# Performance work log

Hardware: AMD Instinct MI355X
Metric: run time of the kernel (lower is better)

Reference implementation:

```python
import jax, jax.numpy as jnp
import numpy as np

B, N, C, D = 16, 1024, 768, 384

def setup_inputs() -> dict:
    key = jax.random.key(0)
    ks = jax.random.split(key, 12)
    s_in = 1.0 / np.sqrt(C)
    s_d = 1.0 / np.sqrt(D)
    return {
        "x": jax.random.normal(ks[0], (B, N, C), dtype=jnp.float32),
        "adj": jax.random.uniform(ks[1], (B, N, N), dtype=jnp.float32),
        "W_theta": jax.random.uniform(ks[2], (C, D), minval=-s_in, maxval=s_in),
        "b_theta": jax.random.uniform(ks[3], (D,), minval=-s_in, maxval=s_in),
        "W_phi": jax.random.uniform(ks[4], (C, D), minval=-s_in, maxval=s_in),
        "b_phi": jax.random.uniform(ks[5], (D,), minval=-s_in, maxval=s_in),
        "W_g": jax.random.uniform(ks[6], (C, D), minval=-s_in, maxval=s_in),
        "b_g": jax.random.uniform(ks[7], (D,), minval=-s_in, maxval=s_in),
        "W_out": jax.random.uniform(ks[8], (D, C), minval=-s_d, maxval=s_d),
        "b_out": jax.random.uniform(ks[9], (C,), minval=-s_d, maxval=s_d),
    }

def reference(x, adj, W_theta, b_theta, W_phi, b_phi, W_g, b_g, W_out, b_out):
    # projections: [B,N,C] @ [C,D] -> [B,N,D]
    theta = x @ W_theta + b_theta
    phi = x @ W_phi + b_phi
    g = x @ W_g + b_g
    # unscaled attention scores with multiplicative adjacency mask
    attn = jnp.einsum('bnd,bmd->bnm', theta, phi) * adj  # [B,N,N]
    attn = jax.nn.softmax(attn, axis=-1)  # dropout is identity in eval mode
    out = jnp.einsum('bnm,bmd->bnd', attn, g)  # [B,N,D]
    out = out @ W_out + b_out  # [B,N,C]
    return out + x
```

## Files before the change

### kernel.cpp

```cpp
#include <hip/hip_runtime.h>
#include <hip/hip_bf16.h>

typedef __hip_bfloat16 bf16;
typedef short bf16x8 __attribute__((ext_vector_type(8)));
typedef float f32x4 __attribute__((ext_vector_type(4)));

constexpr int Bb = 16, Nn = 1024, Cc = 768, Dd = 384;

static __device__ __forceinline__ f32x4 mfma16(bf16x8 a, bf16x8 b, f32x4 c) {
    return __builtin_amdgcn_mfma_f32_16x16x32_bf16(a, b, c, 0, 0, 0);
}
static __device__ __forceinline__ short f2b(float v) {
    __hip_bfloat16 h = __float2bfloat16(v);
    return *reinterpret_cast<short*>(&h);
}
static __device__ __forceinline__ float b2f(bf16 x) { return __bfloat162float(x); }
static __device__ __forceinline__ float ldf(const float* p) { return *p; }
static __device__ __forceinline__ float ldf(const bf16* p) { return __bfloat162float(*p); }

__global__ __launch_bounds__(256) void transpose_cast(
    const float* __restrict__ in, bf16* __restrict__ out, int K, int N)
{
    __shared__ float t[32][33];
    const int n0 = blockIdx.x * 32, k0 = blockIdx.y * 32;
    const int tx = threadIdx.x & 31, ty = threadIdx.x >> 5;
#pragma unroll
    for (int i = 0; i < 4; i++)
        t[ty + i * 8][tx] = in[(size_t)(k0 + ty + i * 8) * N + n0 + tx];
    __syncthreads();
#pragma unroll
    for (int i = 0; i < 4; i++)
        out[(size_t)(n0 + ty + i * 8) * K + k0 + tx] = __float2bfloat16(t[tx][ty + i * 8]);
}

template <typename TA, int EPI>
__global__ __launch_bounds__(256) void gemm_mfma(
    const TA* __restrict__ A, const bf16* __restrict__ BT,
    const float* __restrict__ bias, const float* __restrict__ resid,
    void* __restrict__ outp, int K, int Nout)
{
    __shared__ short As[128 * 40];
    __shared__ short Bs[128 * 40];
    const int tid = threadIdx.x;
    const int lane = tid & 63, w = tid >> 6;
    const int quad = lane >> 4, c = lane & 15;
    const int row0 = blockIdx.x * 128, col0 = blockIdx.y * 128;
    const int wm = (w & 1) * 64, wn = (w >> 1) * 64;

    const f32x4 fz = {0.f, 0.f, 0.f, 0.f};
    f32x4 acc[4][4];
#pragma unroll
    for (int i = 0; i < 4; i++)
#pragma unroll
        for (int j = 0; j < 4; j++) acc[i][j] = fz;

    for (int k0 = 0; k0 < K; k0 += 32) {
        __syncthreads();
        if (sizeof(TA) == 4) {
            const float* Af = (const float*)A;
#pragma unroll
            for (int u = 0; u < 4; u++) {
                const int id = u * 256 + tid;
                const int r = id >> 3, c4 = (id & 7) * 4;
                const float4 v = *reinterpret_cast<const float4*>(Af + (size_t)(row0 + r) * K + k0 + c4);
                uint2 p;
                p.x = ((unsigned)(unsigned short)f2b(v.y) << 16) | (unsigned short)(unsigned)f2b(v.x);
                p.y = ((unsigned)(unsigned short)f2b(v.w) << 16) | (unsigned short)(unsigned)f2b(v.z);
                *reinterpret_cast<uint2*>(&As[r * 40 + c4]) = p;
            }
        } else {
            const bf16* Ab = (const bf16*)A;
#pragma unroll
            for (int u = 0; u < 2; u++) {
                const int id = u * 256 + tid;
                const int r = id >> 2, c8 = (id & 3) * 8;
                const uint4 v = *reinterpret_cast<const uint4*>(Ab + (size_t)(row0 + r) * K + k0 + c8);
                *reinterpret_cast<uint4*>(&As[r * 40 + c8]) = v;
            }
        }
#pragma unroll
        for (int u = 0; u < 2; u++) {
            const int id = u * 256 + tid;
            const int r = id >> 2, c8 = (id & 3) * 8;
            const uint4 v = *reinterpret_cast<const uint4*>(BT + (size_t)(col0 + r) * K + k0 + c8);
            *reinterpret_cast<uint4*>(&Bs[r * 40 + c8]) = v;
        }
        __syncthreads();

        bf16x8 af[4], bfr[4];
#pragma unroll
        for (int i = 0; i < 4; i++)
            af[i] = *reinterpret_cast<const bf16x8*>(&As[(wm + i * 16 + c) * 40 + quad * 8]);
#pragma unroll
        for (int j = 0; j < 4; j++)
            bfr[j] = *reinterpret_cast<const bf16x8*>(&Bs[(wn + j * 16 + c) * 40 + quad * 8]);
#pragma unroll
        for (int i = 0; i < 4; i++)
#pragma unroll
            for (int j = 0; j < 4; j++)
                acc[i][j] = mfma16(af[i], bfr[j], acc[i][j]);
    }

#pragma unroll
    for (int i = 0; i < 4; i++) {
        const int rowb = row0 + wm + i * 16 + quad * 4;
#pragma unroll
        for (int j = 0; j < 4; j++) {
            const int col = col0 + wn + j * 16 + c;
            const float bcol = bias[col];
#pragma unroll
            for (int r = 0; r < 4; r++) {
                float v = acc[i][j][r] + bcol;
                const int rr = rowb + r;
                if (EPI == 0) {
                    ((bf16*)outp)[(size_t)rr * Nout + col] = __float2bfloat16(v);
                } else if (EPI == 1) {
                    const int bb = rr >> 10, m = rr & 1023;
                    ((bf16*)outp)[((size_t)(bb * Nout + col)) * 1024 + m] = __float2bfloat16(v);
                } else {
                    v += resid[(size_t)rr * Nout + col];
                    ((float*)outp)[(size_t)rr * Nout + col] = v;
                }
            }
        }
    }
}

__global__ __launch_bounds__(256) void flash_attn(
    const bf16* __restrict__ theta, const bf16* __restrict__ phi,
    const bf16* __restrict__ gT, const float* __restrict__ adj,
    bf16* __restrict__ O)
{
    __shared__ short phs[32 * 392];
    __shared__ short gts[384 * 40];
    __shared__ short pls[4][16 * 40];

    const int tid = threadIdx.x;
    const int lane = tid & 63, w = tid >> 6;
    const int quad = lane >> 4, c = lane & 15;
    const int qb = blockIdx.x, b = blockIdx.y;

    const size_t thbase = ((size_t)b * Nn + qb * 64 + w * 16 + c) * Dd;
    bf16x8 ath[12];
#pragma unroll
    for (int dq = 0; dq < 12; dq++)
        ath[dq] = *reinterpret_cast<const bf16x8*>(theta + thbase + dq * 32 + quad * 8);

    const f32x4 fz = {0.f, 0.f, 0.f, 0.f};
    f32x4 o[24];
#pragma unroll
    for (int t = 0; t < 24; t++) o[t] = fz;
    float mrow[4], lrow[4];
#pragma unroll
    for (int r = 0; r < 4; r++) { mrow[r] = -INFINITY; lrow[r] = 0.f; }

    for (int n0 = 0; n0 < Nn; n0 += 32) {
        __syncthreads();
        {
            const bf16* src = phi + ((size_t)b * Nn + n0) * Dd;
#pragma unroll
            for (int u = 0; u < 6; u++) {
                const int id = u * 256 + tid;
                const int r = id / 48, cc = (id % 48) * 8;
                const uint4 v = *reinterpret_cast<const uint4*>(src + (size_t)r * Dd + cc);
                *reinterpret_cast<uint4*>(&phs[r * 392 + cc]) = v;
            }
        }
        {
            const bf16* src = gT + ((size_t)b * Dd) * Nn + n0;
#pragma unroll
            for (int u = 0; u < 6; u++) {
                const int id = u * 256 + tid;
                const int r = id >> 2, cc = (id & 3) * 8;
                const uint4 v = *reinterpret_cast<const uint4*>(src + (size_t)r * Nn + cc);
                *reinterpret_cast<uint4*>(&gts[r * 40 + cc]) = v;
            }
        }
        __syncthreads();

        f32x4 s0 = fz, s1 = fz;
#pragma unroll
        for (int dq = 0; dq < 12; dq++) {
            const bf16x8 b0 = *reinterpret_cast<const bf16x8*>(&phs[c * 392 + dq * 32 + quad * 8]);
            const bf16x8 b1 = *reinterpret_cast<const bf16x8*>(&phs[(16 + c) * 392 + dq * 32 + quad * 8]);
            s0 = mfma16(ath[dq], b0, s0);
            s1 = mfma16(ath[dq], b1, s1);
        }

        const float* arow = adj + ((size_t)b * Nn + qb * 64 + w * 16 + quad * 4) * Nn + n0;
        float p0[4], p1[4], alpha[4];
#pragma unroll
        for (int r = 0; r < 4; r++) {
            const float v0 = s0[r] * arow[(size_t)r * Nn + c];
            const float v1 = s1[r] * arow[(size_t)r * Nn + 16 + c];
            float t = fmaxf(v0, v1);
#pragma unroll
            for (int msk = 1; msk < 16; msk <<= 1) t = fmaxf(t, __shfl_xor(t, msk));
            const float mn = fmaxf(mrow[r], t);
            alpha[r] = __expf(mrow[r] - mn);
            mrow[r] = mn;
            p0[r] = __expf(v0 - mn);
            p1[r] = __expf(v1 - mn);
            float u = p0[r] + p1[r];
#pragma unroll
            for (int msk = 1; msk < 16; msk <<= 1) u += __shfl_xor(u, msk);
            lrow[r] = lrow[r] * alpha[r] + u;
        }
#pragma unroll
        for (int t = 0; t < 24; t++)
#pragma unroll
            for (int r = 0; r < 4; r++) o[t][r] *= alpha[r];

        short* pl = (short*)pls[w];
#pragma unroll
        for (int r = 0; r < 4; r++) {
            pl[(quad * 4 + r) * 40 + c] = f2b(p0[r]);
            pl[(quad * 4 + r) * 40 + 16 + c] = f2b(p1[r]);
        }
        __syncthreads();
        const bf16x8 ap = *reinterpret_cast<const bf16x8*>(&pl[c * 40 + quad * 8]);
#pragma unroll
        for (int dn = 0; dn < 24; dn++) {
            const bf16x8 bg = *reinterpret_cast<const bf16x8*>(&gts[(dn * 16 + c) * 40 + quad * 8]);
            o[dn] = mfma16(ap, bg, o[dn]);
        }
    }

    float inv[4];
#pragma unroll
    for (int r = 0; r < 4; r++) inv[r] = 1.0f / lrow[r];
    bf16* orow = O + ((size_t)b * Nn + qb * 64 + w * 16 + quad * 4) * Dd;
#pragma unroll
    for (int dn = 0; dn < 24; dn++)
#pragma unroll
        for (int r = 0; r < 4; r++)
            orow[(size_t)r * Dd + dn * 16 + c] = __float2bfloat16(o[dn][r] * inv[r]);
}

__global__ __launch_bounds__(256) void proj_gemm(
    const float* __restrict__ A, const float* __restrict__ W,
    const float* __restrict__ bias, bf16* __restrict__ out,
    int M, int K, int Nd)
{
    __shared__ float Asm[16][65];
    __shared__ float Bsm[16][65];
    const int tid = threadIdx.x;
    const int tx = tid & 15, ty = tid >> 4;
    const int row0 = blockIdx.x * 64, col0 = blockIdx.y * 64;
    float acc[4][4] = {};
    for (int k0 = 0; k0 < K; k0 += 16) {
        {
            const int m = tid >> 2, kq = (tid & 3) * 4;
            const float* p = A + (size_t)(row0 + m) * K + k0 + kq;
#pragma unroll
            for (int j = 0; j < 4; j++) Asm[kq + j][m] = p[j];
        }
        {
            const int k = tid >> 4, n4 = (tid & 15) * 4;
            const float* p = W + (size_t)(k0 + k) * Nd + col0 + n4;
#pragma unroll
            for (int j = 0; j < 4; j++) Bsm[k][n4 + j] = p[j];
        }
        __syncthreads();
#pragma unroll
        for (int k = 0; k < 16; k++) {
            float a[4], bv[4];
#pragma unroll
            for (int j = 0; j < 4; j++) a[j] = Asm[k][ty * 4 + j];
#pragma unroll
            for (int j = 0; j < 4; j++) bv[j] = Bsm[k][tx * 4 + j];
#pragma unroll
            for (int i = 0; i < 4; i++)
#pragma unroll
                for (int j = 0; j < 4; j++) acc[i][j] += a[i] * bv[j];
        }
        __syncthreads();
    }
#pragma unroll
    for (int i = 0; i < 4; i++) {
        const int row = row0 + ty * 4 + i;
#pragma unroll
        for (int j = 0; j < 4; j++) {
            const int col = col0 + tx * 4 + j;
            out[(size_t)row * Nd + col] = __float2bfloat16(acc[i][j] + bias[col]);
        }
    }
}

__global__ __launch_bounds__(256) void fused_attn(
    const float* __restrict__ x, const float* __restrict__ adj,
    const float* __restrict__ W_theta, const float* __restrict__ b_theta,
    const bf16* __restrict__ phi, const bf16* __restrict__ g,
    const float* __restrict__ W_out, const float* __restrict__ b_out,
    float* __restrict__ out)
{
    __shared__ float xs[Cc];
    __shared__ float th[Dd];
    __shared__ float s[Nn];
    __shared__ float Os[Dd];
    __shared__ float red[256];
    const int tid = threadIdx.x;
    const int n = blockIdx.x, b = blockIdx.y;
    const int lane = tid & 63, wave = tid >> 6;
    const size_t row = (size_t)b * Nn + n;
    const size_t baseD = (size_t)b * Nn * Dd;
    for (int c = tid; c < Cc; c += 256) xs[c] = x[row * Cc + c];
    __syncthreads();
    for (int d = tid; d < Dd; d += 256) {
        float acc = b_theta[d];
#pragma unroll 8
        for (int c = 0; c < Cc; c++) acc += xs[c] * W_theta[(size_t)c * Dd + d];
        th[d] = acc;
    }
    __syncthreads();
    for (int m = wave; m < Nn; m += 4) {
        const bf16* prow = phi + baseD + (size_t)m * Dd;
        float partial = 0.f;
#pragma unroll
        for (int j = 0; j < 6; j++) {
            const int d = lane + 64 * j;
            partial += th[d] * b2f(prow[d]);
        }
#pragma unroll
        for (int off = 32; off > 0; off >>= 1) partial += __shfl_down(partial, off);
        if (lane == 0)
            s[m] = partial * adj[(size_t)b * Nn * Nn + (size_t)n * Nn + m];
    }
    __syncthreads();
    float mx = -1e30f;
    for (int i = tid; i < Nn; i += 256) mx = fmaxf(mx, s[i]);
    red[tid] = mx; __syncthreads();
    for (int st = 128; st > 0; st >>= 1) {
        if (tid < st) red[tid] = fmaxf(red[tid], red[tid + st]);
        __syncthreads();
    }
    mx = red[0]; __syncthreads();
    float lsum = 0.f;
    for (int i = tid; i < Nn; i += 256) {
        const float e = __expf(s[i] - mx);
        s[i] = e;
        lsum += e;
    }
    red[tid] = lsum; __syncthreads();
    for (int st = 128; st > 0; st >>= 1) {
        if (tid < st) red[tid] += red[tid + st];
        __syncthreads();
    }
    const float inv = 1.0f / red[0];
    __syncthreads();
    for (int d = tid; d < Dd; d += 256) {
        float acc = 0.f;
#pragma unroll 8
        for (int m = 0; m < Nn; m++) acc += s[m] * b2f(g[baseD + (size_t)m * Dd + d]);
        Os[d] = acc * inv;
    }
    __syncthreads();
    for (int c = tid; c < Cc; c += 256) {
        float acc = b_out[c] + xs[c];
#pragma unroll 8
        for (int d = 0; d < Dd; d++) acc += Os[d] * W_out[(size_t)d * Cc + c];
        out[row * Cc + c] = acc;
    }
}

extern "C" void kernel_launch(void* const* d_in, const int* in_sizes, int n_in,
                              void* d_out, int out_size, void* d_ws, size_t ws_size,
                              hipStream_t stream)
{
    const float* x       = (const float*)d_in[0];
    const float* adj     = (const float*)d_in[1];
    const float* W_theta = (const float*)d_in[2];
    const float* b_theta = (const float*)d_in[3];
    const float* W_phi   = (const float*)d_in[4];
    const float* b_phi   = (const float*)d_in[5];
    const float* W_g     = (const float*)d_in[6];
    const float* b_g     = (const float*)d_in[7];
    const float* W_out   = (const float*)d_in[8];
    const float* b_out   = (const float*)d_in[9];
    float* out = (float*)d_out;

    const int M = Bb * Nn;
    const size_t SZ = (size_t)Bb * Nn * Dd;
    const size_t WSZ = (size_t)Cc * Dd;
    const size_t NEED = (4 * WSZ + 4 * SZ) * sizeof(bf16);

    dim3 blk(256);

    if (ws_size >= NEED) {
        bf16* WtT   = (bf16*)d_ws;
        bf16* WpT   = WtT + WSZ;
        bf16* WgT   = WpT + WSZ;
        bf16* WoT   = WgT + WSZ;
        bf16* theta = WoT + WSZ;
        bf16* phi   = theta + SZ;
        bf16* gT    = phi + SZ;
        bf16* O     = gT + SZ;

        transpose_cast<<<dim3(Dd / 32, Cc / 32), blk, 0, stream>>>(W_theta, WtT, Cc, Dd);
        transpose_cast<<<dim3(Dd / 32, Cc / 32), blk, 0, stream>>>(W_phi,   WpT, Cc, Dd);
        transpose_cast<<<dim3(Dd / 32, Cc / 32), blk, 0, stream>>>(W_g,     WgT, Cc, Dd);
        transpose_cast<<<dim3(Cc / 32, Dd / 32), blk, 0, stream>>>(W_out,   WoT, Dd, Cc);

        dim3 gp(M / 128, Dd / 128);
        gemm_mfma<float, 0><<<gp, blk, 0, stream>>>(x, WtT, b_theta, nullptr, theta, Cc, Dd);
        gemm_mfma<float, 0><<<gp, blk, 0, stream>>>(x, WpT, b_phi,   nullptr, phi,   Cc, Dd);
        gemm_mfma<float, 1><<<gp, blk, 0, stream>>>(x, WgT, b_g,     nullptr, gT,    Cc, Dd);

        flash_attn<<<dim3(Nn / 64, Bb), blk, 0, stream>>>(theta, phi, gT, adj, O);

        dim3 go(M / 128, Cc / 128);
        gemm_mfma<bf16, 2><<<go, blk, 0, stream>>>(O, WoT, b_out, x, out, Dd, Cc);
    } else {
        bf16* phi = (bf16*)d_ws;
        bf16* g   = phi + SZ;
        dim3 gproj(M / 64, Dd / 64);
        proj_gemm<<<gproj, blk, 0, stream>>>(x, W_phi, b_phi, phi, M, Cc, Dd);
        proj_gemm<<<gproj, blk, 0, stream>>>(x, W_g, b_g, g, M, Cc, Dd);
        fused_attn<<<dim3(Nn, Bb), blk, 0, stream>>>(
            x, adj, W_theta, b_theta, phi, g, W_out, b_out, out);
    }
}
```

Baseline: 377.2 us.

## Fuse projections, double-buffer phi via async LDS loads, read gT from global

The three projection GEMMs become one launch over a concatenated 1152-wide weight, so x is read and converted once, and the three weight transposes become one launch. In attention, phi tiles are double-buffered in LDS with swizzled direct global-to-LDS loads, and adj is loaded before the score MFMAs. The gT tile staging and one barrier per iteration are dropped, so gT is read straight from global memory. The O output overwrites theta in place and the fallback path is removed, which assumes the workspace is always large enough.

```diff
diff --git a/kernel.cpp b/kernel.cpp
--- a/kernel.cpp
+++ b/kernel.cpp
@@ -14,37 +14,57 @@
     __hip_bfloat16 h = __float2bfloat16(v);
     return *reinterpret_cast<short*>(&h);
 }
-static __device__ __forceinline__ float b2f(bf16 x) { return __bfloat162float(x); }
-static __device__ __forceinline__ float ldf(const float* p) { return *p; }
-static __device__ __forceinline__ float ldf(const bf16* p) { return __bfloat162float(*p); }
-
-__global__ __launch_bounds__(256) void transpose_cast(
-    const float* __restrict__ in, bf16* __restrict__ out, int K, int N)
+static __device__ __forceinline__ void ld16(void* lds, const void* g) {
+    __builtin_amdgcn_global_load_lds(
+        (const __attribute__((address_space(1))) unsigned int*)g,
+        (__attribute__((address_space(3))) unsigned int*)lds, 16, 0, 0);
+}
+
+__global__ __launch_bounds__(256) void transpose_proj(
+    const float* __restrict__ W0, const float* __restrict__ W1,
+    const float* __restrict__ W2, bf16* __restrict__ out)
+{
+    __shared__ float t[32][33];
+    const float* in = blockIdx.z == 0 ? W0 : blockIdx.z == 1 ? W1 : W2;
+    bf16* o = out + (size_t)blockIdx.z * Dd * Cc;
+    const int n0 = blockIdx.x * 32, k0 = blockIdx.y * 32;
+    const int tx = threadIdx.x & 31, ty = threadIdx.x >> 5;
+#pragma unroll
+    for (int i = 0; i < 4; i++)
+        t[ty + i * 8][tx] = in[(size_t)(k0 + ty + i * 8) * Dd + n0 + tx];
+    __syncthreads();
+#pragma unroll
+    for (int i = 0; i < 4; i++)
+        o[(size_t)(n0 + ty + i * 8) * Cc + k0 + tx] = __float2bfloat16(t[tx][ty + i * 8]);
+}
+
+__global__ __launch_bounds__(256) void transpose_wout(
+    const float* __restrict__ in, bf16* __restrict__ out)
 {
     __shared__ float t[32][33];
     const int n0 = blockIdx.x * 32, k0 = blockIdx.y * 32;
     const int tx = threadIdx.x & 31, ty = threadIdx.x >> 5;
 #pragma unroll
     for (int i = 0; i < 4; i++)
-        t[ty + i * 8][tx] = in[(size_t)(k0 + ty + i * 8) * N + n0 + tx];
+        t[ty + i * 8][tx] = in[(size_t)(k0 + ty + i * 8) * Cc + n0 + tx];
     __syncthreads();
 #pragma unroll
     for (int i = 0; i < 4; i++)
-        out[(size_t)(n0 + ty + i * 8) * K + k0 + tx] = __float2bfloat16(t[tx][ty + i * 8]);
-}
-
-template <typename TA, int EPI>
-__global__ __launch_bounds__(256) void gemm_mfma(
-    const TA* __restrict__ A, const bf16* __restrict__ BT,
-    const float* __restrict__ bias, const float* __restrict__ resid,
-    void* __restrict__ outp, int K, int Nout)
+        out[(size_t)(n0 + ty + i * 8) * Dd + k0 + tx] = __float2bfloat16(t[tx][ty + i * 8]);
+}
+
+__global__ __launch_bounds__(256) void gemm_proj(
+    const float* __restrict__ A, const bf16* __restrict__ BT,
+    const float* __restrict__ b_t, const float* __restrict__ b_p,
+    const float* __restrict__ b_gv,
+    bf16* __restrict__ th, bf16* __restrict__ ph, bf16* __restrict__ gt)
 {
     __shared__ short As[128 * 40];
     __shared__ short Bs[128 * 40];
     const int tid = threadIdx.x;
     const int lane = tid & 63, w = tid >> 6;
     const int quad = lane >> 4, c = lane & 15;
-    const int row0 = blockIdx.x * 128, col0 = blockIdx.y * 128;
+    const int col0 = blockIdx.x * 128, row0 = blockIdx.y * 128;
     const int wm = (w & 1) * 64, wn = (w >> 1) * 64;
 
     const f32x4 fz = {0.f, 0.f, 0.f, 0.f};
@@ -54,35 +74,100 @@
 #pragma unroll
         for (int j = 0; j < 4; j++) acc[i][j] = fz;
 
-    for (int k0 = 0; k0 < K; k0 += 32) {
-        __syncthreads();
-        if (sizeof(TA) == 4) {
-            const float* Af = (const float*)A;
-#pragma unroll
-            for (int u = 0; u < 4; u++) {
-                const int id = u * 256 + tid;
-                const int r = id >> 3, c4 = (id & 7) * 4;
-                const float4 v = *reinterpret_cast<const float4*>(Af + (size_t)(row0 + r) * K + k0 + c4);
-                uint2 p;
-                p.x = ((unsigned)(unsigned short)f2b(v.y) << 16) | (unsigned short)(unsigned)f2b(v.x);
-                p.y = ((unsigned)(unsigned short)f2b(v.w) << 16) | (unsigned short)(unsigned)f2b(v.z);
-                *reinterpret_cast<uint2*>(&As[r * 40 + c4]) = p;
-            }
-        } else {
-            const bf16* Ab = (const bf16*)A;
-#pragma unroll
-            for (int u = 0; u < 2; u++) {
-                const int id = u * 256 + tid;
-                const int r = id >> 2, c8 = (id & 3) * 8;
-                const uint4 v = *reinterpret_cast<const uint4*>(Ab + (size_t)(row0 + r) * K + k0 + c8);
-                *reinterpret_cast<uint4*>(&As[r * 40 + c8]) = v;
-            }
+    for (int k0 = 0; k0 < Cc; k0 += 32) {
+        __syncthreads();
+#pragma unroll
+        for (int u = 0; u < 4; u++) {
+            const int id = u * 256 + tid;
+            const int r = id >> 3, c4 = (id & 7) * 4;
+            const float4 v = *reinterpret_cast<const float4*>(A + (size_t)(row0 + r) * Cc + k0 + c4);
+            uint2 p;
+            p.x = ((unsigned)(unsigned short)f2b(v.y) << 16) | (unsigned short)(unsigned)f2b(v.x);
+            p.y = ((unsigned)(unsigned short)f2b(v.w) << 16) | (unsigned short)(unsigned)f2b(v.z);
+            *reinterpret_cast<uint2*>(&As[r * 40 + c4]) = p;
         }
 #pragma unroll
         for (int u = 0; u < 2; u++) {
             const int id = u * 256 + tid;
             const int r = id >> 2, c8 = (id & 3) * 8;
-            const uint4 v = *reinterpret_cast<const uint4*>(BT + (size_t)(col0 + r) * K + k0 + c8);
+            const uint4 v = *reinterpret_cast<const uint4*>(BT + (size_t)(col0 + r) * Cc + k0 + c8);
+            *reinterpret_cast<uint4*>(&Bs[r * 40 + c8]) = v;
+        }
+        __syncthreads();
+
+        bf16x8 af[4], bfr[4];
+#pragma unroll
+        for (int i = 0; i < 4; i++)
+            af[i] = *reinterpret_cast<const bf16x8*>(&As[(wm + i * 16 + c) * 40 + quad * 8]);
+#pragma unroll
+        for (int j = 0; j < 4; j++)
+            bfr[j] = *reinterpret_cast<const bf16x8*>(&Bs[(wn + j * 16 + c) * 40 + quad * 8]);
+#pragma unroll
+        for (int i = 0; i < 4; i++)
+#pragma unroll
+            for (int j = 0; j < 4; j++)
+                acc[i][j] = mfma16(af[i], bfr[j], acc[i][j]);
+    }
+
+    const int sel = col0 >= 768 ? 2 : (col0 >= 384 ? 1 : 0);
+    const float* bp = sel == 0 ? b_t : sel == 1 ? b_p : b_gv;
+    bf16* dst = sel == 0 ? th : sel == 1 ? ph : gt;
+    const int cbase = sel * 384;
+#pragma unroll
+    for (int i = 0; i < 4; i++) {
+        const int rowb = row0 + wm + i * 16 + quad * 4;
+#pragma unroll
+        for (int j = 0; j < 4; j++) {
+            const int col = col0 + wn + j * 16 + c;
+            const int cl = col - cbase;
+            const float bcol = bp[cl];
+#pragma unroll
+            for (int r = 0; r < 4; r++) {
+                const float v = acc[i][j][r] + bcol;
+                const int rr = rowb + r;
+                if (sel < 2)
+                    dst[(size_t)rr * 384 + cl] = __float2bfloat16(v);
+                else
+                    dst[((size_t)((rr >> 10) * 384 + cl) << 10) + (rr & 1023)] = __float2bfloat16(v);
+            }
+        }
+    }
+}
+
+__global__ __launch_bounds__(256) void gemm_out(
+    const bf16* __restrict__ A, const bf16* __restrict__ BT,
+    const float* __restrict__ bias, const float* __restrict__ resid,
+    float* __restrict__ out)
+{
+    __shared__ short As[128 * 40];
+    __shared__ short Bs[128 * 40];
+    const int tid = threadIdx.x;
+    const int lane = tid & 63, w = tid >> 6;
+    const int quad = lane >> 4, c = lane & 15;
+    const int col0 = blockIdx.x * 128, row0 = blockIdx.y * 128;
+    const int wm = (w & 1) * 64, wn = (w >> 1) * 64;
+
+    const f32x4 fz = {0.f, 0.f, 0.f, 0.f};
+    f32x4 acc[4][4];
+#pragma unroll
+    for (int i = 0; i < 4; i++)
+#pragma unroll
+        for (int j = 0; j < 4; j++) acc[i][j] = fz;
+
+    for (int k0 = 0; k0 < Dd; k0 += 32) {
+        __syncthreads();
+#pragma unroll
+        for (int u = 0; u < 2; u++) {
+            const int id = u * 256 + tid;
+            const int r = id >> 2, c8 = (id & 3) * 8;
+            const uint4 v = *reinterpret_cast<const uint4*>(A + (size_t)(row0 + r) * Dd + k0 + c8);
+            *reinterpret_cast<uint4*>(&As[r * 40 + c8]) = v;
+        }
+#pragma unroll
+        for (int u = 0; u < 2; u++) {
+            const int id = u * 256 + tid;
+            const int r = id >> 2, c8 = (id & 3) * 8;
+            const uint4 v = *reinterpret_cast<const uint4*>(BT + (size_t)(col0 + r) * Dd + k0 + c8);
             *reinterpret_cast<uint4*>(&Bs[r * 40 + c8]) = v;
         }
         __syncthreads();
@@ -110,29 +195,18 @@
             const float bcol = bias[col];
 #pragma unroll
             for (int r = 0; r < 4; r++) {
-                float v = acc[i][j][r] + bcol;
                 const int rr = rowb + r;
-                if (EPI == 0) {
-                    ((bf16*)outp)[(size_t)rr * Nout + col] = __float2bfloat16(v);
-                } else if (EPI == 1) {
-                    const int bb = rr >> 10, m = rr & 1023;
-                    ((bf16*)outp)[((size_t)(bb * Nout + col)) * 1024 + m] = __float2bfloat16(v);
-                } else {
-                    v += resid[(size_t)rr * Nout + col];
-                    ((float*)outp)[(size_t)rr * Nout + col] = v;
-                }
+                out[(size_t)rr * Cc + col] = acc[i][j][r] + bcol + resid[(size_t)rr * Cc + col];
             }
         }
     }
 }
 
-__global__ __launch_bounds__(256) void flash_attn(
-    const bf16* __restrict__ theta, const bf16* __restrict__ phi,
-    const bf16* __restrict__ gT, const float* __restrict__ adj,
-    bf16* __restrict__ O)
-{
-    __shared__ short phs[32 * 392];
-    __shared__ short gts[384 * 40];
+__global__ __launch_bounds__(256) void flash_attn2(
+    bf16* __restrict__ thetaO, const bf16* __restrict__ phi,
+    const bf16* __restrict__ gT, const float* __restrict__ adj)
+{
+    __shared__ char phs[2][24576];
     __shared__ short pls[4][16 * 40];
 
     const int tid = threadIdx.x;
@@ -140,11 +214,14 @@
     const int quad = lane >> 4, c = lane & 15;
     const int qb = blockIdx.x, b = blockIdx.y;
 
+    const bf16* phi_b = phi + (size_t)b * Nn * Dd;
+    const bf16* gT_b  = gT + (size_t)b * Dd * Nn;
+
     const size_t thbase = ((size_t)b * Nn + qb * 64 + w * 16 + c) * Dd;
     bf16x8 ath[12];
 #pragma unroll
     for (int dq = 0; dq < 12; dq++)
-        ath[dq] = *reinterpret_cast<const bf16x8*>(theta + thbase + dq * 32 + quad * 8);
+        ath[dq] = *reinterpret_cast<const bf16x8*>(thetaO + thbase + dq * 32 + quad * 8);
 
     const f32x4 fz = {0.f, 0.f, 0.f, 0.f};
     f32x4 o[24];
@@ -154,45 +231,56 @@
 #pragma unroll
     for (int r = 0; r < 4; r++) { mrow[r] = -INFINITY; lrow[r] = 0.f; }
 
-    for (int n0 = 0; n0 < Nn; n0 += 32) {
-        __syncthreads();
-        {
-            const bf16* src = phi + ((size_t)b * Nn + n0) * Dd;
-#pragma unroll
-            for (int u = 0; u < 6; u++) {
-                const int id = u * 256 + tid;
-                const int r = id / 48, cc = (id % 48) * 8;
-                const uint4 v = *reinterpret_cast<const uint4*>(src + (size_t)r * Dd + cc);
-                *reinterpret_cast<uint4*>(&phs[r * 392 + cc]) = v;
-            }
-        }
-        {
-            const bf16* src = gT + ((size_t)b * Dd) * Nn + n0;
-#pragma unroll
-            for (int u = 0; u < 6; u++) {
-                const int id = u * 256 + tid;
-                const int r = id >> 2, cc = (id & 3) * 8;
-                const uint4 v = *reinterpret_cast<const uint4*>(src + (size_t)r * Nn + cc);
-                *reinterpret_cast<uint4*>(&gts[r * 40 + cc]) = v;
-            }
-        }
-        __syncthreads();
+    {
+        char* dst = phs[0];
+#pragma unroll
+        for (int t = 0; t < 6; t++) {
+            const int op = w * 6 + t;
+            const int gc = op * 64 + lane;
+            const int r = gc / 48, j = gc - r * 48;
+            ld16(dst + op * 1024, phi_b + (size_t)r * Dd + ((j ^ (r & 7)) << 3));
+        }
+    }
+
+    for (int ci = 0; ci < 32; ci++) {
+        const int n0 = ci * 32;
+        __syncthreads();
+        const char* buf = phs[ci & 1];
+
+        const float* arow = adj + ((size_t)b * Nn + qb * 64 + w * 16 + quad * 4) * Nn + n0;
+        float a0[4], a1[4];
+#pragma unroll
+        for (int r = 0; r < 4; r++) {
+            a0[r] = arow[(size_t)r * Nn + c];
+            a1[r] = arow[(size_t)r * Nn + 16 + c];
+        }
 
         f32x4 s0 = fz, s1 = fz;
 #pragma unroll
         for (int dq = 0; dq < 12; dq++) {
-            const bf16x8 b0 = *reinterpret_cast<const bf16x8*>(&phs[c * 392 + dq * 32 + quad * 8]);
-            const bf16x8 b1 = *reinterpret_cast<const bf16x8*>(&phs[(16 + c) * 392 + dq * 32 + quad * 8]);
+            const int sw = ((dq * 4 + quad) ^ (c & 7)) << 4;
+            const bf16x8 b0 = *reinterpret_cast<const bf16x8*>(buf + c * 768 + sw);
+            const bf16x8 b1 = *reinterpret_cast<const bf16x8*>(buf + (16 + c) * 768 + sw);
             s0 = mfma16(ath[dq], b0, s0);
             s1 = mfma16(ath[dq], b1, s1);
         }
 
-        const float* arow = adj + ((size_t)b * Nn + qb * 64 + w * 16 + quad * 4) * Nn + n0;
+        if (ci < 31) {
+            char* dst = phs[(ci + 1) & 1];
+#pragma unroll
+            for (int t = 0; t < 6; t++) {
+                const int op = w * 6 + t;
+                const int gc = op * 64 + lane;
+                const int r = gc / 48, j = gc - r * 48;
+                ld16(dst + op * 1024, phi_b + (size_t)(n0 + 32 + r) * Dd + ((j ^ (r & 7)) << 3));
+            }
+        }
+
         float p0[4], p1[4], alpha[4];
 #pragma unroll
         for (int r = 0; r < 4; r++) {
-            const float v0 = s0[r] * arow[(size_t)r * Nn + c];
-            const float v1 = s1[r] * arow[(size_t)r * Nn + 16 + c];
+            const float v0 = s0[r] * a0[r];
+            const float v1 = s1[r] * a1[r];
             float t = fmaxf(v0, v1);
 #pragma unroll
             for (int msk = 1; msk < 16; msk <<= 1) t = fmaxf(t, __shfl_xor(t, msk));
@@ -217,11 +305,12 @@
             pl[(quad * 4 + r) * 40 + c] = f2b(p0[r]);
             pl[(quad * 4 + r) * 40 + 16 + c] = f2b(p1[r]);
         }
-        __syncthreads();
         const bf16x8 ap = *reinterpret_cast<const bf16x8*>(&pl[c * 40 + quad * 8]);
+
 #pragma unroll
         for (int dn = 0; dn < 24; dn++) {
-            const bf16x8 bg = *reinterpret_cast<const bf16x8*>(&gts[(dn * 16 + c) * 40 + quad * 8]);
+            const bf16x8 bg = *reinterpret_cast<const bf16x8*>(
+                gT_b + (size_t)(dn * 16 + c) * Nn + n0 + quad * 8);
             o[dn] = mfma16(ap, bg, o[dn]);
         }
     }
@@ -229,138 +318,12 @@
     float inv[4];
 #pragma unroll
     for (int r = 0; r < 4; r++) inv[r] = 1.0f / lrow[r];
-    bf16* orow = O + ((size_t)b * Nn + qb * 64 + w * 16 + quad * 4) * Dd;
+    bf16* orow = thetaO + ((size_t)b * Nn + qb * 64 + w * 16 + quad * 4) * Dd;
 #pragma unroll
     for (int dn = 0; dn < 24; dn++)
 #pragma unroll
         for (int r = 0; r < 4; r++)
             orow[(size_t)r * Dd + dn * 16 + c] = __float2bfloat16(o[dn][r] * inv[r]);
-}
-
-__global__ __launch_bounds__(256) void proj_gemm(
-    const float* __restrict__ A, const float* __restrict__ W,
-    const float* __restrict__ bias, bf16* __restrict__ out,
-    int M, int K, int Nd)
-{
-    __shared__ float Asm[16][65];
-    __shared__ float Bsm[16][65];
-    const int tid = threadIdx.x;
-    const int tx = tid & 15, ty = tid >> 4;
-    const int row0 = blockIdx.x * 64, col0 = blockIdx.y * 64;
-    float acc[4][4] = {};
-    for (int k0 = 0; k0 < K; k0 += 16) {
-        {
-            const int m = tid >> 2, kq = (tid & 3) * 4;
-            const float* p = A + (size_t)(row0 + m) * K + k0 + kq;
-#pragma unroll
-            for (int j = 0; j < 4; j++) Asm[kq + j][m] = p[j];
-        }
-        {
-            const int k = tid >> 4, n4 = (tid & 15) * 4;
-            const float* p = W + (size_t)(k0 + k) * Nd + col0 + n4;
-#pragma unroll
-            for (int j = 0; j < 4; j++) Bsm[k][n4 + j] = p[j];
-        }
-        __syncthreads();
-#pragma unroll
-        for (int k = 0; k < 16; k++) {
-            float a[4], bv[4];
-#pragma unroll
-            for (int j = 0; j < 4; j++) a[j] = Asm[k][ty * 4 + j];
-#pragma unroll
-            for (int j = 0; j < 4; j++) bv[j] = Bsm[k][tx * 4 + j];
-#pragma unroll
-            for (int i = 0; i < 4; i++)
-#pragma unroll
-                for (int j = 0; j < 4; j++) acc[i][j] += a[i] * bv[j];
-        }
-        __syncthreads();
-    }
-#pragma unroll
-    for (int i = 0; i < 4; i++) {
-        const int row = row0 + ty * 4 + i;
-#pragma unroll
-        for (int j = 0; j < 4; j++) {
-            const int col = col0 + tx * 4 + j;
-            out[(size_t)row * Nd + col] = __float2bfloat16(acc[i][j] + bias[col]);
-        }
-    }
-}
-
-__global__ __launch_bounds__(256) void fused_attn(
-    const float* __restrict__ x, const float* __restrict__ adj,
-    const float* __restrict__ W_theta, const float* __restrict__ b_theta,
-    const bf16* __restrict__ phi, const bf16* __restrict__ g,
-    const float* __restrict__ W_out, const float* __restrict__ b_out,
-    float* __restrict__ out)
-{
-    __shared__ float xs[Cc];
-    __shared__ float th[Dd];
-    __shared__ float s[Nn];
-    __shared__ float Os[Dd];
-    __shared__ float red[256];
-    const int tid = threadIdx.x;
-    const int n = blockIdx.x, b = blockIdx.y;
-    const int lane = tid & 63, wave = tid >> 6;
-    const size_t row = (size_t)b * Nn + n;
-    const size_t baseD = (size_t)b * Nn * Dd;
-    for (int c = tid; c < Cc; c += 256) xs[c] = x[row * Cc + c];
-    __syncthreads();
-    for (int d = tid; d < Dd; d += 256) {
-        float acc = b_theta[d];
-#pragma unroll 8
-        for (int c = 0; c < Cc; c++) acc += xs[c] * W_theta[(size_t)c * Dd + d];
-        th[d] = acc;
-    }
-    __syncthreads();
-    for (int m = wave; m < Nn; m += 4) {
-        const bf16* prow = phi + baseD + (size_t)m * Dd;
-        float partial = 0.f;
-#pragma unroll
-        for (int j = 0; j < 6; j++) {
-            const int d = lane + 64 * j;
-            partial += th[d] * b2f(prow[d]);
-        }
-#pragma unroll
-        for (int off = 32; off > 0; off >>= 1) partial += __shfl_down(partial, off);
-        if (lane == 0)
-            s[m] = partial * adj[(size_t)b * Nn * Nn + (size_t)n * Nn + m];
-    }
-    __syncthreads();
-    float mx = -1e30f;
-    for (int i = tid; i < Nn; i += 256) mx = fmaxf(mx, s[i]);
-    red[tid] = mx; __syncthreads();
-    for (int st = 128; st > 0; st >>= 1) {
-        if (tid < st) red[tid] = fmaxf(red[tid], red[tid + st]);
-        __syncthreads();
-    }
-    mx = red[0]; __syncthreads();
-    float lsum = 0.f;
-    for (int i = tid; i < Nn; i += 256) {
-        const float e = __expf(s[i] - mx);
-        s[i] = e;
-        lsum += e;
-    }
-    red[tid] = lsum; __syncthreads();
-    for (int st = 128; st > 0; st >>= 1) {
-        if (tid < st) red[tid] += red[tid + st];
-        __syncthreads();
-    }
-    const float inv = 1.0f / red[0];
-    __syncthreads();
-    for (int d = tid; d < Dd; d += 256) {
-        float acc = 0.f;
-#pragma unroll 8
-        for (int m = 0; m < Nn; m++) acc += s[m] * b2f(g[baseD + (size_t)m * Dd + d]);
-        Os[d] = acc * inv;
-    }
-    __syncthreads();
-    for (int c = tid; c < Cc; c += 256) {
-        float acc = b_out[c] + xs[c];
-#pragma unroll 8
-        for (int d = 0; d < Dd; d++) acc += Os[d] * W_out[(size_t)d * Cc + c];
-        out[row * Cc + c] = acc;
-    }
 }
 
 extern "C" void kernel_launch(void* const* d_in, const int* in_sizes, int n_in,
@@ -379,44 +342,24 @@
     const float* b_out   = (const float*)d_in[9];
     float* out = (float*)d_out;
 
-    const int M = Bb * Nn;
-    const size_t SZ = (size_t)Bb * Nn * Dd;
+    const size_t SZ  = (size_t)Bb * Nn * Dd;
     const size_t WSZ = (size_t)Cc * Dd;
-    const size_t NEED = (4 * WSZ + 4 * SZ) * sizeof(bf16);
+
+    bf16* WT_all = (bf16*)d_ws;
+    bf16* WoT    = WT_all + 3 * WSZ;
+    bf16* thetaO = WoT + WSZ;
+    bf16* phi    = thetaO + SZ;
+    bf16* gT     = phi + SZ;
 
     dim3 blk(256);
 
-    if (ws_size >= NEED) {
-        bf16* WtT   = (bf16*)d_ws;
-        bf16* WpT   = WtT + WSZ;
-        bf16* WgT   = WpT + WSZ;
-        bf16* WoT   = WgT + WSZ;
-        bf16* theta = WoT + WSZ;
-        bf16* phi   = theta + SZ;
-        bf16* gT    = phi + SZ;
-        bf16* O     = gT + SZ;
-
-        transpose_cast<<<dim3(Dd / 32, Cc / 32), blk, 0, stream>>>(W_theta, WtT, Cc, Dd);
-        transpose_cast<<<dim3(Dd / 32, Cc / 32), blk, 0, stream>>>(W_phi,   WpT, Cc, Dd);
-        transpose_cast<<<dim3(Dd / 32, Cc / 32), blk, 0, stream>>>(W_g,     WgT, Cc, Dd);
-        transpose_cast<<<dim3(Cc / 32, Dd / 32), blk, 0, stream>>>(W_out,   WoT, Dd, Cc);
-
-        dim3 gp(M / 128, Dd / 128);
-        gemm_mfma<float, 0><<<gp, blk, 0, stream>>>(x, WtT, b_theta, nullptr, theta, Cc, Dd);
-        gemm_mfma<float, 0><<<gp, blk, 0, stream>>>(x, WpT, b_phi,   nullptr, phi,   Cc, Dd);
-        gemm_mfma<float, 1><<<gp, blk, 0, stream>>>(x, WgT, b_g,     nullptr, gT,    Cc, Dd);
-
-        flash_attn<<<dim3(Nn / 64, Bb), blk, 0, stream>>>(theta, phi, gT, adj, O);
-
-        dim3 go(M / 128, Cc / 128);
-        gemm_mfma<bf16, 2><<<go, blk, 0, stream>>>(O, WoT, b_out, x, out, Dd, Cc);
-    } else {
-        bf16* phi = (bf16*)d_ws;
-        bf16* g   = phi + SZ;
-        dim3 gproj(M / 64, Dd / 64);
-        proj_gemm<<<gproj, blk, 0, stream>>>(x, W_phi, b_phi, phi, M, Cc, Dd);
-        proj_gemm<<<gproj, blk, 0, stream>>>(x, W_g, b_g, g, M, Cc, Dd);
-        fused_attn<<<dim3(Nn, Bb), blk, 0, stream>>>(
-            x, adj, W_theta, b_theta, phi, g, W_out, b_out, out);
-    }
-}
+    transpose_proj<<<dim3(12, 24, 3), blk, 0, stream>>>(W_theta, W_phi, W_g, WT_all);
+    transpose_wout<<<dim3(24, 12), blk, 0, stream>>>(W_out, WoT);
+
+    gemm_proj<<<dim3(9, 128), blk, 0, stream>>>(
+        x, WT_all, b_theta, b_phi, b_g, thetaO, phi, gT);
+
+    flash_attn2<<<dim3(Nn / 64, Bb), blk, 0, stream>>>(thetaO, phi, gT, adj);
+
+    gemm_out<<<dim3(6, 128), blk, 0, stream>>>(thetaO, WoT, b_out, x, out);
+}
```

After: 428.3 us. 13.5% more time.
